# Optimization experiments

Hardware: AMD Instinct MI355X
Metric: run time of the kernel (lower is better)

Reference implementation:

```python
import jax, jax.numpy as jnp
import numpy as np

N, M, D = 16384, 8192, 3
ATOM_DIMS, CHEM, K = 6, 16, 16
GAMMA = 1.0
BIG = 1e10


def _leaky(x):
    return jax.nn.leaky_relu(x, negative_slope=0.2)


def _linear(x, W, b=None):
    # torch nn.Linear: y = x @ W.T + b, W: [out, in]
    y = x @ W.T
    return y if b is None else y + b


def setup_inputs() -> dict:
    key = jax.random.key(0)
    ks = jax.random.split(key, 16)

    def lin(k, out_d, in_d):
        bound = 1.0 / np.sqrt(in_d)
        k1, k2 = jax.random.split(k)
        W = jax.random.uniform(k1, (out_d, in_d), minval=-bound, maxval=bound, dtype=jnp.float32)
        b = jax.random.uniform(k2, (out_d,), minval=-bound, maxval=bound, dtype=jnp.float32)
        return W, b

    W_t1, b_t1 = lin(ks[0], CHEM, ATOM_DIMS)
    W_t2, b_t2 = lin(ks[1], CHEM, CHEM)
    W_t3, b_t3 = lin(ks[2], CHEM, CHEM)
    W_att = jax.random.uniform(ks[3], (1, K), minval=-1.0 / np.sqrt(K), maxval=1.0 / np.sqrt(K), dtype=jnp.float32)
    W_e1, b_e1 = lin(ks[4], CHEM, CHEM)
    W_e2, b_e2 = lin(ks[5], CHEM, CHEM)
    W_e3, b_e3 = lin(ks[6], CHEM, CHEM)

    return {
        "xyz": jax.random.normal(ks[7], (N, D), dtype=jnp.float32) * 10.0,
        "atom_xyz": jax.random.normal(ks[8], (M, D), dtype=jnp.float32) * 10.0,
        "atomtypes": jax.random.uniform(ks[9], (M, ATOM_DIMS), dtype=jnp.float32),
        "batch": jnp.zeros((N,), dtype=jnp.int64),
        "atom_batch": jnp.zeros((M,), dtype=jnp.int64),
        "W_t1": W_t1, "b_t1": b_t1, "W_t2": W_t2, "b_t2": b_t2, "W_t3": W_t3, "b_t3": b_t3,
        "W_att": W_att,
        "W_e1": W_e1, "b_e1": b_e1, "W_e2": W_e2, "b_e2": b_e2, "W_e3": W_e3, "b_e3": b_e3,
    }


def reference(xyz, atom_xyz, atomtypes, batch, atom_batch,
              W_t1, b_t1, W_t2, b_t2, W_t3, b_t3, W_att,
              W_e1, b_e1, W_e2, b_e2, W_e3, b_e3):
    # transform_types MLP on atom one-hots -> [M, CHEM]
    t = atomtypes[:, :ATOM_DIMS]
    t = _leaky(_linear(t, W_t1, b_t1))
    t = _leaky(_linear(t, W_t2, b_t2))
    t = _leaky(_linear(t, W_t3, b_t3))

    # batched kNN: squared distances [N, M], cross-batch pairs masked out
    d2 = (jnp.sum(xyz * xyz, -1)[:, None] + jnp.sum(atom_xyz * atom_xyz, -1)[None, :]
          - 2.0 * (xyz @ atom_xyz.T))
    d2 = jnp.where(batch[:, None] == atom_batch[None, :], d2, BIG)
    _, idx = jax.lax.top_k(-d2, K)  # idx: [N, K] nearest atoms

    x_ik = atom_xyz[idx]                       # [N, K, 3]
    vecs = xyz[:, None, :] - x_ik              # [N, K, 3]
    dists = jnp.sum(vecs * vecs, -1)           # [N, K]
    w = jnp.power(dists + 1e-8, -(1.0 + GAMMA) / 2.0)
    norm_vec = vecs * w[:, :, None]            # [N, K, 3]
    feat = t[idx]                              # [N, K, CHEM]

    # outer product [N, K, 3, C] transposed to [N, C, 3, K], attention Linear over K,
    # fused into one einsum (dropout is identity at eval)
    fx = jnp.einsum('nkd,nkc,k->ncd', norm_vec, feat, W_att[0])  # [N, C, 3]
    fx = jnp.sqrt(jnp.sum(fx * fx, -1))        # [N, C]

    fx = _leaky(_linear(fx, W_e1, b_e1))
    fx = _leaky(_linear(fx, W_e2, b_e2))
    fx = _linear(fx, W_e3, b_e3)
    return fx
```

## Files before the change

### kernel.cpp

```cpp
#include <hip/hip_runtime.h>
#include <cfloat>

#define NPTS   16384
#define MATOMS 8192
#define CH     16
#define ADIM   6
#define KNN    16
#define GROUPS_PER_BLOCK 8
#define PTSPG  2
#define BIGF   1e10f
#define SLOTS  16
#define CHUNK  512
#define NCHUNK (MATOMS/CHUNK)
#define VMINC  4
#define NPASS  (VMINC + NCHUNK)

__device__ __forceinline__ float leakyf(float x) { return x >= 0.0f ? x : 0.2f * x; }

__global__ void __launch_bounds__(256) prep_kernel(
    const float* __restrict__ atom_xyz,
    const float* __restrict__ atomtypes,
    const int*   __restrict__ atom_batch,
    const float* __restrict__ Wt1, const float* __restrict__ bt1,
    const float* __restrict__ Wt2, const float* __restrict__ bt2,
    const float* __restrict__ Wt3, const float* __restrict__ bt3,
    float4* __restrict__ pos4,
    float*  __restrict__ tbuf,
    int*    __restrict__ abatch)
{
    __shared__ float w1[CH*ADIM], w2[CH*CH], w3[CH*CH], bb1[CH], bb2[CH], bb3[CH];
    const int tid = threadIdx.x;
    if (tid < CH*ADIM) w1[tid] = Wt1[tid];
    if (tid < CH*CH)   { w2[tid] = Wt2[tid]; w3[tid] = Wt3[tid]; }
    if (tid < CH)      { bb1[tid] = bt1[tid]; bb2[tid] = bt2[tid]; bb3[tid] = bt3[tid]; }
    __syncthreads();
    const int m = blockIdx.x * 256 + tid;
    if (m >= MATOMS) return;

    float x[ADIM];
    #pragma unroll
    for (int j = 0; j < ADIM; ++j) x[j] = atomtypes[m*ADIM + j];

    float h0[CH], h1[CH], h2[CH];
    #pragma unroll
    for (int c = 0; c < CH; ++c) {
        float a = 0.0f;
        #pragma unroll
        for (int j = 0; j < ADIM; ++j) a = fmaf(w1[c*ADIM+j], x[j], a);
        h0[c] = leakyf(a + bb1[c]);
    }
    #pragma unroll
    for (int c = 0; c < CH; ++c) {
        float a = 0.0f;
        #pragma unroll
        for (int j = 0; j < CH; ++j) a = fmaf(w2[c*CH+j], h0[j], a);
        h1[c] = leakyf(a + bb2[c]);
    }
    #pragma unroll
    for (int c = 0; c < CH; ++c) {
        float a = 0.0f;
        #pragma unroll
        for (int j = 0; j < CH; ++j) a = fmaf(w3[c*CH+j], h1[j], a);
        h2[c] = leakyf(a + bb3[c]);
    }
    #pragma unroll
    for (int c = 0; c < CH; ++c) tbuf[m*CH + c] = h2[c];

    const float ax = atom_xyz[m*3+0], ay = atom_xyz[m*3+1], az = atom_xyz[m*3+2];
    const float a2 = __fadd_rn(__fadd_rn(__fmul_rn(ax,ax), __fmul_rn(ay,ay)), __fmul_rn(az,az));
    pos4[m] = make_float4(ax, ay, az, a2);
    abatch[m] = atom_batch[m];
}

__device__ __forceinline__ void knn_select(
    int c32, float px, float py, float pz, float pn2, int pb,
    int skip, int cnt, const unsigned short* seg,
    const float4* __restrict__ pos4, const int* __restrict__ abatch,
    float bd[KNN], int bi[KNN])
{
    int ovf = skip | (cnt > SLOTS);
    ovf |= __shfl_xor(ovf, 1);
    ovf |= __shfl_xor(ovf, 2);
    ovf |= __shfl_xor(ovf, 4);
    ovf |= __shfl_xor(ovf, 8);
    ovf |= __shfl_xor(ovf, 16);

    #pragma unroll
    for (int j = 0; j < KNN; ++j) { bd[j] = FLT_MAX; bi[j] = 0x7fffffff; }

    if (ovf) {
        for (int t = 0; t < MATOMS/32; ++t) {
            const int i = t*32 + c32;
            const float4 a = pos4[i];
            const int ab = abatch[i];
            const float dot = fmaf(pz, a.z, fmaf(py, a.y, __fmul_rn(px, a.x)));
            float d2 = __fsub_rn(__fadd_rn(pn2, a.w), 2.0f * dot);
            d2 = (ab == pb) ? d2 : BIGF;
            if (d2 < bd[KNN-1]) {
                float d = d2; int id = i;
                #pragma unroll
                for (int j = 0; j < KNN; ++j) {
                    const bool sw = d < bd[j];
                    const float od = bd[j]; const int oi = bi[j];
                    bd[j] = sw ? d  : bd[j];
                    bi[j] = sw ? id : bi[j];
                    d  = sw ? od : d;
                    id = sw ? oi : id;
                }
            }
        }
    } else {
        for (int s = 0; s < cnt; ++s) {
            const int i = (int)seg[s*32];
            const float4 a = pos4[i];
            const float dot = fmaf(pz, a.z, fmaf(py, a.y, __fmul_rn(px, a.x)));
            const float d2 = __fsub_rn(__fadd_rn(pn2, a.w), 2.0f * dot);
            if (abatch[i] == pb && d2 <= bd[KNN-1]) {
                float d = d2; int id = i;
                #pragma unroll
                for (int j = 0; j < KNN; ++j) {
                    const bool sw = (d < bd[j]) || (d == bd[j] && id < bi[j]);
                    const float od = bd[j]; const int oi = bi[j];
                    bd[j] = sw ? d  : bd[j];
                    bi[j] = sw ? id : bi[j];
                    d  = sw ? od : d;
                    id = sw ? oi : id;
                }
            }
        }
    }
}

__device__ __forceinline__ void knn_merge2(
    float* bd0, int* bi0, float* bd1, int* bi1,
    int* idxk0, int* idxk1)
{
    #pragma unroll
    for (int k = 0; k < KNN; ++k) {
        float d0 = bd0[0]; int i0 = bi0[0];
        float d1 = bd1[0]; int i1 = bi1[0];
        #pragma unroll
        for (int m = 1; m <= 16; m <<= 1) {
            const float pd0 = __shfl_xor(d0, m);
            const int   pi0 = __shfl_xor(i0, m);
            const float pd1 = __shfl_xor(d1, m);
            const int   pi1 = __shfl_xor(i1, m);
            const bool t0 = (pd0 < d0) || (pd0 == d0 && pi0 < i0);
            const bool t1 = (pd1 < d1) || (pd1 == d1 && pi1 < i1);
            d0 = t0 ? pd0 : d0;
            i0 = t0 ? pi0 : i0;
            d1 = t1 ? pd1 : d1;
            i1 = t1 ? pi1 : i1;
        }
        idxk0[k] = i0;
        idxk1[k] = i1;
        const bool w0 = (bd0[0] == d0) && (bi0[0] == i0);
        const bool w1 = (bd1[0] == d1) && (bi1[0] == i1);
        if (w0) {
            #pragma unroll
            for (int j = 0; j < KNN-1; ++j) { bd0[j] = bd0[j+1]; bi0[j] = bi0[j+1]; }
            bd0[KNN-1] = FLT_MAX; bi0[KNN-1] = 0x7fffffff;
        }
        if (w1) {
            #pragma unroll
            for (int j = 0; j < KNN-1; ++j) { bd1[j] = bd1[j+1]; bi1[j] = bi1[j+1]; }
            bd1[KNN-1] = FLT_MAX; bi1[KNN-1] = 0x7fffffff;
        }
    }
}

__global__ void __launch_bounds__(256) atom_main_kernel(
    const float* __restrict__ xyz,
    const int*   __restrict__ batch,
    const float4* __restrict__ pos4,
    const float* __restrict__ tbuf,
    const int*   __restrict__ abatch,
    const float* __restrict__ Watt,
    const float* __restrict__ We1, const float* __restrict__ be1,
    const float* __restrict__ We2, const float* __restrict__ be2,
    const float* __restrict__ We3, const float* __restrict__ be3,
    float* __restrict__ out)
{
    __shared__ float lw1t[CH*CH], lw2t[CH*CH], lw3t[CH*CH];
    __shared__ float lb1[CH], lb2[CH], lb3[CH], lwatt[KNN];
    __shared__ unsigned short lbuf[GROUPS_PER_BLOCK * PTSPG * SLOTS * 32];
    __shared__ float4 lpos[2][CHUNK];
    const int tid = threadIdx.x;
    lw1t[tid] = We1[(tid & 15)*CH + (tid >> 4)];
    lw2t[tid] = We2[(tid & 15)*CH + (tid >> 4)];
    lw3t[tid] = We3[(tid & 15)*CH + (tid >> 4)];
    if (tid < CH) { lb1[tid] = be1[tid]; lb2[tid] = be2[tid]; lb3[tid] = be3[tid]; lwatt[tid] = Watt[tid]; }

    const int c32 = tid & 31;
    const int grp = tid >> 5;
    const int n0  = (blockIdx.x * GROUPS_PER_BLOCK + grp) * PTSPG;
    const int n1  = n0 + 1;

    const float px0 = xyz[n0*3+0], py0 = xyz[n0*3+1], pz0 = xyz[n0*3+2];
    const float px1 = xyz[n1*3+0], py1 = xyz[n1*3+1], pz1 = xyz[n1*3+2];
    const float pn20 = __fadd_rn(__fadd_rn(__fmul_rn(px0,px0), __fmul_rn(py0,py0)), __fmul_rn(pz0,pz0));
    const float pn21 = __fadd_rn(__fadd_rn(__fmul_rn(px1,px1), __fmul_rn(py1,py1)), __fmul_rn(pz1,pz1));
    const int pb0 = batch[n0];
    const int pb1 = batch[n1];

    {
        const float4 q0 = pos4[tid];
        const float4 q1 = pos4[tid+256];
        lpos[0][tid]     = make_float4(-2.0f*q0.x, -2.0f*q0.y, -2.0f*q0.z, q0.w);
        lpos[0][tid+256] = make_float4(-2.0f*q1.x, -2.0f*q1.y, -2.0f*q1.z, q1.w);
    }

    float vmin0 = FLT_MAX, vmin1 = FLT_MAX;
    float tauf0 = 0.0f, tauf1 = 0.0f;
    int   skip0 = 0, skip1 = 0;
    int   cnt0 = 0, cnt1 = 0;
    unsigned short* seg0 = &lbuf[(grp*PTSPG + 0) * (SLOTS*32) + c32];
    unsigned short* seg1 = &lbuf[(grp*PTSPG + 1) * (SLOTS*32) + c32];

    for (int g = 0; g < NPASS; ++g) {
        const int cur = g & 1;
        __syncthreads();
        float4 q0, q1;
        const bool pf = (g+1 < NPASS);
        if (pf) {
            const int nc = (g+1 < VMINC) ? (g+1) : (g+1-VMINC);
            const int base = nc*CHUNK;
            q0 = pos4[base+tid]; q1 = pos4[base+tid+256];
        }
        if (g == VMINC) {
            float tau0 = FLT_MAX, tau1 = FLT_MAX;
            {
                float v = vmin0;
                #pragma unroll
                for (int k = 0; k < KNN; ++k) {
                    float d = v;
                    d = fminf(d, __shfl_xor(d, 1));
                    d = fminf(d, __shfl_xor(d, 2));
                    d = fminf(d, __shfl_xor(d, 4));
                    d = fminf(d, __shfl_xor(d, 8));
                    d = fminf(d, __shfl_xor(d, 16));
                    tau0 = d;
                    if (v == d) v = FLT_MAX;
                }
            }
            {
                float v = vmin1;
                #pragma unroll
                for (int k = 0; k < KNN; ++k) {
                    float d = v;
                    d = fminf(d, __shfl_xor(d, 1));
                    d = fminf(d, __shfl_xor(d, 2));
                    d = fminf(d, __shfl_xor(d, 4));
                    d = fminf(d, __shfl_xor(d, 8));
                    d = fminf(d, __shfl_xor(d, 16));
                    tau1 = d;
                    if (v == d) v = FLT_MAX;
                }
            }
            skip0 = !(tau0 < BIGF);
            skip1 = !(tau1 < BIGF);
            tauf0 = skip0 ? -FLT_MAX : tau0 + (1e-5f*(fabsf(pn20) + fabsf(tau0)) + 1e-2f);
            tauf1 = skip1 ? -FLT_MAX : tau1 + (1e-5f*(fabsf(pn21) + fabsf(tau1)) + 1e-2f);
        }
        if (g < VMINC) {
            #pragma unroll 4
            for (int t = 0; t < CHUNK/32; ++t) {
                const int il = t*32 + c32;
                const float4 a = lpos[cur][il];
                const float lhs0 = fmaf(pz0, a.z, fmaf(py0, a.y, fmaf(px0, a.x, a.w)));
                const float lhs1 = fmaf(pz1, a.z, fmaf(py1, a.y, fmaf(px1, a.x, a.w)));
                if (lhs0 < vmin0) { if (abatch[g*CHUNK + il] == pb0) vmin0 = lhs0; }
                if (lhs1 < vmin1) { if (abatch[g*CHUNK + il] == pb1) vmin1 = lhs1; }
            }
        } else {
            const int cb = g - VMINC;
            #pragma unroll 4
            for (int t = 0; t < CHUNK/32; ++t) {
                const int il = t*32 + c32;
                const float4 a = lpos[cur][il];
                const float lhs0 = fmaf(pz0, a.z, fmaf(py0, a.y, fmaf(px0, a.x, a.w)));
                const float lhs1 = fmaf(pz1, a.z, fmaf(py1, a.y, fmaf(px1, a.x, a.w)));
                const int gi = cb*CHUNK + il;
                if (lhs0 <= tauf0) {
                    if (cnt0 < SLOTS) seg0[cnt0*32] = (unsigned short)gi;
                    ++cnt0;
                }
                if (lhs1 <= tauf1) {
                    if (cnt1 < SLOTS) seg1[cnt1*32] = (unsigned short)gi;
                    ++cnt1;
                }
            }
        }
        if (pf) {
            lpos[cur^1][tid]     = make_float4(-2.0f*q0.x, -2.0f*q0.y, -2.0f*q0.z, q0.w);
            lpos[cur^1][tid+256] = make_float4(-2.0f*q1.x, -2.0f*q1.y, -2.0f*q1.z, q1.w);
        }
    }

    float bd0[KNN]; int bi0[KNN];
    float bd1[KNN]; int bi1[KNN];
    knn_select(c32, px0, py0, pz0, pn20, pb0, skip0, cnt0, seg0, pos4, abatch, bd0, bi0);
    knn_select(c32, px1, py1, pz1, pn21, pb1, skip1, cnt1, seg1, pos4, abatch, bd1, bi1);

    int idxk0[KNN], idxk1[KNN];
    knn_merge2(bd0, bi0, bd1, bi1, idxk0, idxk1);

    {
        const int half = (tid >> 4) & 1;
        const int c = tid & 15;
        const int myn = half ? n1 : n0;
        const float px = half ? px1 : px0;
        const float py = half ? py1 : py0;
        const float pz = half ? pz1 : pz0;
        int myidx[KNN];
        #pragma unroll
        for (int k = 0; k < KNN; ++k) myidx[k] = half ? idxk1[k] : idxk0[k];

        float ac0 = 0.0f, ac1 = 0.0f, ac2 = 0.0f;
        #pragma unroll
        for (int k = 0; k < KNN; ++k) {
            const int j = myidx[k];
            const float4 a = pos4[j];
            const float v0 = __fsub_rn(px, a.x);
            const float v1 = __fsub_rn(py, a.y);
            const float v2 = __fsub_rn(pz, a.z);
            const float dist = __fadd_rn(__fadd_rn(__fmul_rn(v0,v0), __fmul_rn(v1,v1)), __fmul_rn(v2,v2));
            const float w = 1.0f / __fadd_rn(dist, 1e-8f);
            const float nv0 = __fmul_rn(v0, w);
            const float nv1 = __fmul_rn(v1, w);
            const float nv2 = __fmul_rn(v2, w);
            const float fc = tbuf[(size_t)j * CH + c];
            const float fw = __fmul_rn(fc, lwatt[k]);
            ac0 = fmaf(nv0, fw, ac0);
            ac1 = fmaf(nv1, fw, ac1);
            ac2 = fmaf(nv2, fw, ac2);
        }
        const float s = __fadd_rn(__fadd_rn(__fmul_rn(ac0,ac0), __fmul_rn(ac1,ac1)),
                                  __fmul_rn(ac2,ac2));
        const float fx = sqrtf(s);

        float a1 = 0.0f;
        #pragma unroll
        for (int j = 0; j < CH; ++j) {
            const float fj = __shfl(fx, j, 16);
            a1 = fmaf(lw1t[j*CH + c], fj, a1);
        }
        const float g1 = leakyf(a1 + lb1[c]);

        float a2 = 0.0f;
        #pragma unroll
        for (int j = 0; j < CH; ++j) {
            const float gj = __shfl(g1, j, 16);
            a2 = fmaf(lw2t[j*CH + c], gj, a2);
        }
        const float g2 = leakyf(a2 + lb2[c]);

        float a3 = 0.0f;
        #pragma unroll
        for (int j = 0; j < CH; ++j) {
            const float gj = __shfl(g2, j, 16);
            a3 = fmaf(lw3t[j*CH + c], gj, a3);
        }
        out[(size_t)myn*CH + c] = a3 + lb3[c];
    }
}

extern "C" void kernel_launch(void* const* d_in, const int* in_sizes, int n_in,
                              void* d_out, int out_size, void* d_ws, size_t ws_size,
                              hipStream_t stream)
{
    (void)in_sizes; (void)n_in; (void)out_size; (void)ws_size;
    const float* xyz        = (const float*)d_in[0];
    const float* atom_xyz   = (const float*)d_in[1];
    const float* atomtypes  = (const float*)d_in[2];
    const int*   batch      = (const int*)d_in[3];
    const int*   atom_batch = (const int*)d_in[4];
    const float* Wt1 = (const float*)d_in[5];
    const float* bt1 = (const float*)d_in[6];
    const float* Wt2 = (const float*)d_in[7];
    const float* bt2 = (const float*)d_in[8];
    const float* Wt3 = (const float*)d_in[9];
    const float* bt3 = (const float*)d_in[10];
    const float* Watt = (const float*)d_in[11];
    const float* We1 = (const float*)d_in[12];
    const float* be1 = (const float*)d_in[13];
    const float* We2 = (const float*)d_in[14];
    const float* be2 = (const float*)d_in[15];
    const float* We3 = (const float*)d_in[16];
    const float* be3 = (const float*)d_in[17];

    char* ws = (char*)d_ws;
    float4* pos4  = (float4*)ws;
    float*  tbuf  = (float*)(ws + 131072);
    int*    abat  = (int*)(ws + 131072 + 524288);
    float*  out   = (float*)d_out;

    hipLaunchKernelGGL(prep_kernel, dim3(MATOMS/256), dim3(256), 0, stream,
                       atom_xyz, atomtypes, atom_batch,
                       Wt1, bt1, Wt2, bt2, Wt3, bt3,
                       pos4, tbuf, abat);
    hipLaunchKernelGGL(atom_main_kernel, dim3(NPTS/(GROUPS_PER_BLOCK*PTSPG)), dim3(256), 0, stream,
                       xyz, batch, pos4, tbuf, abat,
                       Watt, We1, be1, We2, be2, We3, be3,
                       out);
}
```

Before: 119.7 us.

## Process four query points per warp group to amortize shared-memory atom loads

Each 32-lane group now handles four query points instead of two, so every atom position read from shared memory is reused for four distance evaluations in both the threshold and candidate-collection passes. The grid shrinks by half, and the kNN select/merge and epilogue run twice per group via new helper functions. This raises register pressure and the shared candidate buffer doubles, which may lower occupancy, and fewer blocks means less parallelism across the GPU. The host launch grid must match the new points-per-block count; that code is not shown.

```diff
diff --git a/kernel.cpp b/kernel.cpp
--- a/kernel.cpp
+++ b/kernel.cpp
@@ -7,7 +7,7 @@
 #define ADIM   6
 #define KNN    16
 #define GROUPS_PER_BLOCK 8
-#define PTSPG  2
+#define PTSPG  4
 #define BIGF   1e10f
 #define SLOTS  16
 #define CHUNK  512
@@ -169,6 +169,92 @@
     }
 }
 
+__device__ __forceinline__ void tau_pair(float vA, float vB, float* tA, float* tB)
+{
+    float a = vA, b = vB;
+    float ta = FLT_MAX, tb = FLT_MAX;
+    #pragma unroll
+    for (int k = 0; k < KNN; ++k) {
+        float da = a, db = b;
+        #pragma unroll
+        for (int m = 1; m <= 16; m <<= 1) {
+            da = fminf(da, __shfl_xor(da, m));
+            db = fminf(db, __shfl_xor(db, m));
+        }
+        ta = da; tb = db;
+        if (a == da) a = FLT_MAX;
+        if (b == db) b = FLT_MAX;
+    }
+    *tA = ta; *tB = tb;
+}
+
+__device__ __forceinline__ void epilogue_pair(
+    int tid, int nA, int nB,
+    float pxA, float pyA, float pzA, float pxB, float pyB, float pzB,
+    const int* idxkA, const int* idxkB,
+    const float4* __restrict__ pos4, const float* __restrict__ tbuf,
+    const float* lwatt, const float* lw1t, const float* lw2t, const float* lw3t,
+    const float* lb1, const float* lb2, const float* lb3,
+    float* __restrict__ out)
+{
+    const int half = (tid >> 4) & 1;
+    const int c = tid & 15;
+    const int myn = half ? nB : nA;
+    const float px = half ? pxB : pxA;
+    const float py = half ? pyB : pyA;
+    const float pz = half ? pzB : pzA;
+    int myidx[KNN];
+    #pragma unroll
+    for (int k = 0; k < KNN; ++k) myidx[k] = half ? idxkB[k] : idxkA[k];
+
+    float ac0 = 0.0f, ac1 = 0.0f, ac2 = 0.0f;
+    #pragma unroll
+    for (int k = 0; k < KNN; ++k) {
+        const int j = myidx[k];
+        const float4 a = pos4[j];
+        const float v0 = __fsub_rn(px, a.x);
+        const float v1 = __fsub_rn(py, a.y);
+        const float v2 = __fsub_rn(pz, a.z);
+        const float dist = __fadd_rn(__fadd_rn(__fmul_rn(v0,v0), __fmul_rn(v1,v1)), __fmul_rn(v2,v2));
+        const float w = 1.0f / __fadd_rn(dist, 1e-8f);
+        const float nv0 = __fmul_rn(v0, w);
+        const float nv1 = __fmul_rn(v1, w);
+        const float nv2 = __fmul_rn(v2, w);
+        const float fc = tbuf[(size_t)j * CH + c];
+        const float fw = __fmul_rn(fc, lwatt[k]);
+        ac0 = fmaf(nv0, fw, ac0);
+        ac1 = fmaf(nv1, fw, ac1);
+        ac2 = fmaf(nv2, fw, ac2);
+    }
+    const float s = __fadd_rn(__fadd_rn(__fmul_rn(ac0,ac0), __fmul_rn(ac1,ac1)),
+                              __fmul_rn(ac2,ac2));
+    const float fx = sqrtf(s);
+
+    float a1 = 0.0f;
+    #pragma unroll
+    for (int j = 0; j < CH; ++j) {
+        const float fj = __shfl(fx, j, 16);
+        a1 = fmaf(lw1t[j*CH + c], fj, a1);
+    }
+    const float g1 = leakyf(a1 + lb1[c]);
+
+    float a2 = 0.0f;
+    #pragma unroll
+    for (int j = 0; j < CH; ++j) {
+        const float gj = __shfl(g1, j, 16);
+        a2 = fmaf(lw2t[j*CH + c], gj, a2);
+    }
+    const float g2 = leakyf(a2 + lb2[c]);
+
+    float a3 = 0.0f;
+    #pragma unroll
+    for (int j = 0; j < CH; ++j) {
+        const float gj = __shfl(g2, j, 16);
+        a3 = fmaf(lw3t[j*CH + c], gj, a3);
+    }
+    out[(size_t)myn*CH + c] = a3 + lb3[c];
+}
+
 __global__ void __launch_bounds__(256) atom_main_kernel(
     const float* __restrict__ xyz,
     const int*   __restrict__ batch,
@@ -195,13 +281,21 @@
     const int grp = tid >> 5;
     const int n0  = (blockIdx.x * GROUPS_PER_BLOCK + grp) * PTSPG;
     const int n1  = n0 + 1;
+    const int n2  = n0 + 2;
+    const int n3  = n0 + 3;
 
     const float px0 = xyz[n0*3+0], py0 = xyz[n0*3+1], pz0 = xyz[n0*3+2];
     const float px1 = xyz[n1*3+0], py1 = xyz[n1*3+1], pz1 = xyz[n1*3+2];
+    const float px2 = xyz[n2*3+0], py2 = xyz[n2*3+1], pz2 = xyz[n2*3+2];
+    const float px3 = xyz[n3*3+0], py3 = xyz[n3*3+1], pz3 = xyz[n3*3+2];
     const float pn20 = __fadd_rn(__fadd_rn(__fmul_rn(px0,px0), __fmul_rn(py0,py0)), __fmul_rn(pz0,pz0));
     const float pn21 = __fadd_rn(__fadd_rn(__fmul_rn(px1,px1), __fmul_rn(py1,py1)), __fmul_rn(pz1,pz1));
+    const float pn22 = __fadd_rn(__fadd_rn(__fmul_rn(px2,px2), __fmul_rn(py2,py2)), __fmul_rn(pz2,pz2));
+    const float pn23 = __fadd_rn(__fadd_rn(__fmul_rn(px3,px3), __fmul_rn(py3,py3)), __fmul_rn(pz3,pz3));
     const int pb0 = batch[n0];
     const int pb1 = batch[n1];
+    const int pb2 = batch[n2];
+    const int pb3 = batch[n3];
 
     {
         const float4 q0 = pos4[tid];
@@ -210,12 +304,14 @@
         lpos[0][tid+256] = make_float4(-2.0f*q1.x, -2.0f*q1.y, -2.0f*q1.z, q1.w);
     }
 
-    float vmin0 = FLT_MAX, vmin1 = FLT_MAX;
-    float tauf0 = 0.0f, tauf1 = 0.0f;
-    int   skip0 = 0, skip1 = 0;
-    int   cnt0 = 0, cnt1 = 0;
+    float vmin0 = FLT_MAX, vmin1 = FLT_MAX, vmin2 = FLT_MAX, vmin3 = FLT_MAX;
+    float tauf0 = 0.0f, tauf1 = 0.0f, tauf2 = 0.0f, tauf3 = 0.0f;
+    int   skip0 = 0, skip1 = 0, skip2 = 0, skip3 = 0;
+    int   cnt0 = 0, cnt1 = 0, cnt2 = 0, cnt3 = 0;
     unsigned short* seg0 = &lbuf[(grp*PTSPG + 0) * (SLOTS*32) + c32];
     unsigned short* seg1 = &lbuf[(grp*PTSPG + 1) * (SLOTS*32) + c32];
+    unsigned short* seg2 = &lbuf[(grp*PTSPG + 2) * (SLOTS*32) + c32];
+    unsigned short* seg3 = &lbuf[(grp*PTSPG + 3) * (SLOTS*32) + c32];
 
     for (int g = 0; g < NPASS; ++g) {
         const int cur = g & 1;
@@ -228,39 +324,17 @@
             q0 = pos4[base+tid]; q1 = pos4[base+tid+256];
         }
         if (g == VMINC) {
-            float tau0 = FLT_MAX, tau1 = FLT_MAX;
-            {
-                float v = vmin0;
-                #pragma unroll
-                for (int k = 0; k < KNN; ++k) {
-                    float d = v;
-                    d = fminf(d, __shfl_xor(d, 1));
-                    d = fminf(d, __shfl_xor(d, 2));
-                    d = fminf(d, __shfl_xor(d, 4));
-                    d = fminf(d, __shfl_xor(d, 8));
-                    d = fminf(d, __shfl_xor(d, 16));
-                    tau0 = d;
-                    if (v == d) v = FLT_MAX;
-                }
-            }
-            {
-                float v = vmin1;
-                #pragma unroll
-                for (int k = 0; k < KNN; ++k) {
-                    float d = v;
-                    d = fminf(d, __shfl_xor(d, 1));
-                    d = fminf(d, __shfl_xor(d, 2));
-                    d = fminf(d, __shfl_xor(d, 4));
-                    d = fminf(d, __shfl_xor(d, 8));
-                    d = fminf(d, __shfl_xor(d, 16));
-                    tau1 = d;
-                    if (v == d) v = FLT_MAX;
-                }
-            }
+            float tau0, tau1, tau2, tau3;
+            tau_pair(vmin0, vmin1, &tau0, &tau1);
+            tau_pair(vmin2, vmin3, &tau2, &tau3);
             skip0 = !(tau0 < BIGF);
             skip1 = !(tau1 < BIGF);
+            skip2 = !(tau2 < BIGF);
+            skip3 = !(tau3 < BIGF);
             tauf0 = skip0 ? -FLT_MAX : tau0 + (1e-5f*(fabsf(pn20) + fabsf(tau0)) + 1e-2f);
             tauf1 = skip1 ? -FLT_MAX : tau1 + (1e-5f*(fabsf(pn21) + fabsf(tau1)) + 1e-2f);
+            tauf2 = skip2 ? -FLT_MAX : tau2 + (1e-5f*(fabsf(pn22) + fabsf(tau2)) + 1e-2f);
+            tauf3 = skip3 ? -FLT_MAX : tau3 + (1e-5f*(fabsf(pn23) + fabsf(tau3)) + 1e-2f);
         }
         if (g < VMINC) {
             #pragma unroll 4
@@ -269,8 +343,12 @@
                 const float4 a = lpos[cur][il];
                 const float lhs0 = fmaf(pz0, a.z, fmaf(py0, a.y, fmaf(px0, a.x, a.w)));
                 const float lhs1 = fmaf(pz1, a.z, fmaf(py1, a.y, fmaf(px1, a.x, a.w)));
+                const float lhs2 = fmaf(pz2, a.z, fmaf(py2, a.y, fmaf(px2, a.x, a.w)));
+                const float lhs3 = fmaf(pz3, a.z, fmaf(py3, a.y, fmaf(px3, a.x, a.w)));
                 if (lhs0 < vmin0) { if (abatch[g*CHUNK + il] == pb0) vmin0 = lhs0; }
                 if (lhs1 < vmin1) { if (abatch[g*CHUNK + il] == pb1) vmin1 = lhs1; }
+                if (lhs2 < vmin2) { if (abatch[g*CHUNK + il] == pb2) vmin2 = lhs2; }
+                if (lhs3 < vmin3) { if (abatch[g*CHUNK + il] == pb3) vmin3 = lhs3; }
             }
         } else {
             const int cb = g - VMINC;
@@ -280,6 +358,8 @@
                 const float4 a = lpos[cur][il];
                 const float lhs0 = fmaf(pz0, a.z, fmaf(py0, a.y, fmaf(px0, a.x, a.w)));
                 const float lhs1 = fmaf(pz1, a.z, fmaf(py1, a.y, fmaf(px1, a.x, a.w)));
+                const float lhs2 = fmaf(pz2, a.z, fmaf(py2, a.y, fmaf(px2, a.x, a.w)));
+                const float lhs3 = fmaf(pz3, a.z, fmaf(py3, a.y, fmaf(px3, a.x, a.w)));
                 const int gi = cb*CHUNK + il;
                 if (lhs0 <= tauf0) {
                     if (cnt0 < SLOTS) seg0[cnt0*32] = (unsigned short)gi;
@@ -289,6 +369,14 @@
                     if (cnt1 < SLOTS) seg1[cnt1*32] = (unsigned short)gi;
                     ++cnt1;
                 }
+                if (lhs2 <= tauf2) {
+                    if (cnt2 < SLOTS) seg2[cnt2*32] = (unsigned short)gi;
+                    ++cnt2;
+                }
+                if (lhs3 <= tauf3) {
+                    if (cnt3 < SLOTS) seg3[cnt3*32] = (unsigned short)gi;
+                    ++cnt3;
+                }
             }
         }
         if (pf) {
@@ -297,72 +385,26 @@
         }
     }
 
-    float bd0[KNN]; int bi0[KNN];
-    float bd1[KNN]; int bi1[KNN];
-    knn_select(c32, px0, py0, pz0, pn20, pb0, skip0, cnt0, seg0, pos4, abatch, bd0, bi0);
-    knn_select(c32, px1, py1, pz1, pn21, pb1, skip1, cnt1, seg1, pos4, abatch, bd1, bi1);
-
-    int idxk0[KNN], idxk1[KNN];
-    knn_merge2(bd0, bi0, bd1, bi1, idxk0, idxk1);
-
+    int idxk0[KNN], idxk1[KNN], idxk2[KNN], idxk3[KNN];
     {
-        const int half = (tid >> 4) & 1;
-        const int c = tid & 15;
-        const int myn = half ? n1 : n0;
-        const float px = half ? px1 : px0;
-        const float py = half ? py1 : py0;
-        const float pz = half ? pz1 : pz0;
-        int myidx[KNN];
-        #pragma unroll
-        for (int k = 0; k < KNN; ++k) myidx[k] = half ? idxk1[k] : idxk0[k];
-
-        float ac0 = 0.0f, ac1 = 0.0f, ac2 = 0.0f;
-        #pragma unroll
-        for (int k = 0; k < KNN; ++k) {
-            const int j = myidx[k];
-            const float4 a = pos4[j];
-            const float v0 = __fsub_rn(px, a.x);
-            const float v1 = __fsub_rn(py, a.y);
-            const float v2 = __fsub_rn(pz, a.z);
-            const float dist = __fadd_rn(__fadd_rn(__fmul_rn(v0,v0), __fmul_rn(v1,v1)), __fmul_rn(v2,v2));
-            const float w = 1.0f / __fadd_rn(dist, 1e-8f);
-            const float nv0 = __fmul_rn(v0, w);
-            const float nv1 = __fmul_rn(v1, w);
-            const float nv2 = __fmul_rn(v2, w);
-            const float fc = tbuf[(size_t)j * CH + c];
-            const float fw = __fmul_rn(fc, lwatt[k]);
-            ac0 = fmaf(nv0, fw, ac0);
-            ac1 = fmaf(nv1, fw, ac1);
-            ac2 = fmaf(nv2, fw, ac2);
-        }
-        const float s = __fadd_rn(__fadd_rn(__fmul_rn(ac0,ac0), __fmul_rn(ac1,ac1)),
-                                  __fmul_rn(ac2,ac2));
-        const float fx = sqrtf(s);
-
-        float a1 = 0.0f;
-        #pragma unroll
-        for (int j = 0; j < CH; ++j) {
-            const float fj = __shfl(fx, j, 16);
-            a1 = fmaf(lw1t[j*CH + c], fj, a1);
-        }
-        const float g1 = leakyf(a1 + lb1[c]);
-
-        float a2 = 0.0f;
-        #pragma unroll
-        for (int j = 0; j < CH; ++j) {
-            const float gj = __shfl(g1, j, 16);
-            a2 = fmaf(lw2t[j*CH + c], gj, a2);
-        }
-        const float g2 = leakyf(a2 + lb2[c]);
-
-        float a3 = 0.0f;
-        #pragma unroll
-        for (int j = 0; j < CH; ++j) {
-            const float gj = __shfl(g2, j, 16);
-            a3 = fmaf(lw3t[j*CH + c], gj, a3);
-        }
-        out[(size_t)myn*CH + c] = a3 + lb3[c];
-    }
+        float bdA[KNN]; int biA[KNN];
+        float bdB[KNN]; int biB[KNN];
+        knn_select(c32, px0, py0, pz0, pn20, pb0, skip0, cnt0, seg0, pos4, abatch, bdA, biA);
+        knn_select(c32, px1, py1, pz1, pn21, pb1, skip1, cnt1, seg1, pos4, abatch, bdB, biB);
+        knn_merge2(bdA, biA, bdB, biB, idxk0, idxk1);
+    }
+    {
+        float bdA[KNN]; int biA[KNN];
+        float bdB[KNN]; int biB[KNN];
+        knn_select(c32, px2, py2, pz2, pn22, pb2, skip2, cnt2, seg2, pos4, abatch, bdA, biA);
+        knn_select(c32, px3, py3, pz3, pn23, pb3, skip3, cnt3, seg3, pos4, abatch, bdB, biB);
+        knn_merge2(bdA, biA, bdB, biB, idxk2, idxk3);
+    }
+
+    epilogue_pair(tid, n0, n1, px0, py0, pz0, px1, py1, pz1, idxk0, idxk1,
+                  pos4, tbuf, lwatt, lw1t, lw2t, lw3t, lb1, lb2, lb3, out);
+    epilogue_pair(tid, n2, n3, px2, py2, pz2, px3, py3, pz3, idxk2, idxk3,
+                  pos4, tbuf, lwatt, lw1t, lw2t, lw3t, lb1, lb2, lb3, out);
 }
 
 extern "C" void kernel_launch(void* const* d_in, const int* in_sizes, int n_in,
```

Result: slower. 176.8 us (+47.7%).
